# Kernel tuning notes

Hardware: AMD Instinct MI355X
Metric: run time of the kernel (lower is better)

Reference implementation:

```python
import jax, jax.numpy as jnp
import numpy as np

B, T, D, U, C = 256, 512, 128, 128, 64


def setup_inputs() -> dict:
    key = jax.random.key(0)
    ks = jax.random.split(key, 4)
    s_in = 1.0 / np.sqrt(D)
    s_u = 1.0 / np.sqrt(U)
    return {
        "inputs": jax.random.normal(ks[0], (B, T, D), dtype=jnp.float32),
        "W1": jax.random.normal(ks[1], (D, U), dtype=jnp.float32) * s_in,
        "b1": jnp.zeros((U,), dtype=jnp.float32),
        "W2": jax.random.normal(ks[2], (U, U), dtype=jnp.float32) * s_u,
        "b2": jnp.zeros((U,), dtype=jnp.float32),
        "Wc": jax.random.normal(ks[3], (U, C), dtype=jnp.float32) * s_u,
        "bc": jnp.zeros((C,), dtype=jnp.float32),
    }


def reference(inputs, W1, b1, W2, b2, Wc, bc):
    # state_{t} = tanh(x_t @ W1 + b1) + tanh(state_{t-1} @ W2 + b2)
    # Input projection has no recurrent dependency -> precompute in one big GEMM.
    h = jnp.tanh(jnp.einsum("btd,du->btu", inputs, W1) + b1)  # (B, T, U)

    def step(state, h_t):
        y = h_t + jnp.tanh(state @ W2 + b2)  # (B, U)
        return y, y

    state0 = jnp.zeros((inputs.shape[0], W2.shape[0]), dtype=inputs.dtype)
    _, ys = jax.lax.scan(step, state0, jnp.swapaxes(h, 0, 1))  # ys: (T, B, U)
    features = jnp.swapaxes(ys, 0, 1)  # (B, T, U)
    # classifier: Dense head applied to stacked features
    return jnp.einsum("btu,uc->btc", features, Wc) + bc
```

## Files before the change

kernel.cpp:

```cpp
#include <hip/hip_runtime.h>

#define NB 256
#define NT 512
#define ND 128
#define NU 128
#define NC 64
#define NM (NB * NT)
#define YP 136

typedef _Float16 half2v __attribute__((ext_vector_type(2)));
typedef _Float16 half4v __attribute__((ext_vector_type(4)));
typedef _Float16 half8v __attribute__((ext_vector_type(8)));
typedef float f32x4 __attribute__((ext_vector_type(4)));
typedef float v2f __attribute__((ext_vector_type(2)));

#define MFMA(a, b, c) __builtin_amdgcn_mfma_f32_16x16x32_f16((a), (b), (c), 0, 0, 0)

__device__ __forceinline__ half2v pk2(float a, float b) {
  return __builtin_bit_cast(half2v, __builtin_amdgcn_cvt_pkrtz(a, b));
}

__device__ __forceinline__ float tanh_s(float s) {
  float e = __expf(s);
  return fmaf(-2.0f, __builtin_amdgcn_rcpf(e + 1.0f), 1.0f);
}

__device__ __forceinline__ void wg_barrier() {
  asm volatile("s_waitcnt lgkmcnt(0)\n\ts_barrier" ::: "memory");
}

__global__ __launch_bounds__(256, 1) void k1_inproj(
    const float* __restrict__ x, const float* __restrict__ W1,
    const float* __restrict__ b1v, _Float16* __restrict__ TH)
{
  __shared__ _Float16 W1T[ND * YP];
  const int tid = (int)threadIdx.x;
  for (int i = tid; i < ND * NU; i += 256) {
    int k = i >> 7, n = i & 127;
    W1T[n * YP + k] = (_Float16)(2.0f * W1[i]);
  }
  __syncthreads();

  const int L = tid & 63, wv = tid >> 6;
  const int v = L & 15, q = L >> 4;
  const int m0 = (int)blockIdx.x * 64 + wv * 16;

  const float* xr = x + (size_t)(m0 + v) * ND + 8 * q;
  half8v xf[4];
#pragma unroll
  for (int kk = 0; kk < 4; ++kk) {
    float4 a = *(const float4*)(xr + 32 * kk);
    float4 b = *(const float4*)(xr + 32 * kk + 4);
    half2v p0 = pk2(a.x, a.y), p1 = pk2(a.z, a.w);
    half2v p2 = pk2(b.x, b.y), p3 = pk2(b.z, b.w);
    xf[kk] = (half8v){p0[0], p0[1], p1[0], p1[1], p2[0], p2[1], p3[0], p3[1]};
  }

#pragma unroll
  for (int ht = 0; ht < 8; ++ht) {
    f32x4 acc;
    {
      float4 bb = *(const float4*)&b1v[16 * ht + 4 * q];
      acc = (f32x4){2.f * bb.x, 2.f * bb.y, 2.f * bb.z, 2.f * bb.w};
    }
#pragma unroll
    for (int kk = 0; kk < 4; ++kk) {
      half8v wa = *(const half8v*)&W1T[(16 * ht + v) * YP + 32 * kk + 8 * q];
      acc = MFMA(wa, xf[kk], acc);
    }
    half2v zlo = pk2(tanh_s(acc[0]), tanh_s(acc[1]));
    half2v zhi = pk2(tanh_s(acc[2]), tanh_s(acc[3]));
    half4v z = {zlo[0], zlo[1], zhi[0], zhi[1]};
    *(half4v*)&TH[(size_t)(m0 + v) * NU + 16 * ht + 4 * q] = z;
  }
}

__global__ __launch_bounds__(512, 1) void k2_recur(
    const _Float16* __restrict__ TH, const float* __restrict__ W2,
    const float* __restrict__ b2v, _Float16* __restrict__ Yws)
{
  __shared__ _Float16 Ybuf[2][16 * YP];

  const int tid = (int)threadIdx.x;
  const int w = tid >> 6;
  const int L = tid & 63;
  const int v = L & 15, q = L >> 4;
  const int b0 = (int)blockIdx.x * 16;

  half8v w2f[4];
#pragma unroll
  for (int kk = 0; kk < 4; ++kk) {
    half8v h;
#pragma unroll
    for (int j = 0; j < 8; ++j)
      h[j] = (_Float16)(2.0f * W2[(size_t)(32 * kk + 8 * q + j) * NU + 16 * w + v]);
    w2f[kk] = h;
  }
  f32x4 b2f;
  {
    float4 bb = *(const float4*)&b2v[16 * w + 4 * q];
    b2f = (f32x4){2.f * bb.x, 2.f * bb.y, 2.f * bb.z, 2.f * bb.w};
  }

  const _Float16* thp = TH + (size_t)(b0 + v) * NT * NU + 16 * w + 4 * q;
  _Float16* yp = Yws + (size_t)(b0 + v) * NT * NU + 16 * w + 4 * q;

  half4v thr0 = *(const half4v*)(thp + 0 * NU);
  half4v thr1 = *(const half4v*)(thp + 1 * NU);
  half4v thr2 = *(const half4v*)(thp + 2 * NU);
  half4v thr3 = *(const half4v*)(thp + 3 * NU);

  f32x4 racc = b2f;
  _Float16* wr = &Ybuf[0][0] + v * YP + 16 * w + 4 * q;
  const _Float16* rd = &Ybuf[0][0] + v * YP + 8 * q;

#define K2STEP(T_, THR_, BUF_)                                                \
  {                                                                           \
    const int t_ = (T_);                                                      \
    half2v zlo = pk2(tanh_s(racc[0]), tanh_s(racc[1]));                       \
    half2v zhi = pk2(tanh_s(racc[2]), tanh_s(racc[3]));                       \
    half2v tlo = __builtin_shufflevector(THR_, THR_, 0, 1);                   \
    half2v thi = __builtin_shufflevector(THR_, THR_, 2, 3);                   \
    half2v ylo = zlo + tlo;                                                   \
    half2v yhi = zhi + thi;                                                   \
    half4v y4 = {ylo[0], ylo[1], yhi[0], yhi[1]};                             \
    *(half4v*)(wr + (BUF_) * (16 * YP)) = y4;                                 \
    *(half4v*)(yp + (size_t)t_ * NU) = y4;         \
    {                                                                         \
      int tn = t_ + 4; tn = tn < NT ? tn : NT - 1;                            \
      THR_ = *(const half4v*)(thp + (size_t)tn * NU);                         \
    }                                                                         \
    wg_barrier();                                                             \
    half8v yf0 = *(const half8v*)(rd + (BUF_) * (16 * YP) + 0);               \
    half8v yf1 = *(const half8v*)(rd + (BUF_) * (16 * YP) + 32);              \
    half8v yf2 = *(const half8v*)(rd + (BUF_) * (16 * YP) + 64);              \
    half8v yf3 = *(const half8v*)(rd + (BUF_) * (16 * YP) + 96);              \
    racc = b2f;                                                               \
    racc = MFMA(w2f[0], yf0, racc);                                           \
    racc = MFMA(w2f[1], yf1, racc);                                           \
    racc = MFMA(w2f[2], yf2, racc);                                           \
    racc = MFMA(w2f[3], yf3, racc);                                           \
  }

#pragma unroll 1
  for (int t = 0; t < NT; t += 4) {
    K2STEP(t + 0, thr0, 0)
    K2STEP(t + 1, thr1, 1)
    K2STEP(t + 2, thr2, 0)
    K2STEP(t + 3, thr3, 1)
  }
}

__global__ __launch_bounds__(256, 1) void k3_head(
    const _Float16* __restrict__ Y, const float* __restrict__ Wc,
    const float* __restrict__ bcv, float* __restrict__ out)
{
  __shared__ _Float16 WcT[NC * YP];
  const int tid = (int)threadIdx.x;
  for (int i = tid; i < NU * NC; i += 256) {
    int k = i >> 6, c = i & 63;
    WcT[c * YP + k] = (_Float16)Wc[i];
  }
  __syncthreads();

  const int L = tid & 63, wv = tid >> 6;
  const int v = L & 15, q = L >> 4;
  const int m0 = (int)blockIdx.x * 64 + wv * 16;

  const _Float16* yr = Y + (size_t)(m0 + v) * NU + 8 * q;
  half8v yf[4];
#pragma unroll
  for (int kk = 0; kk < 4; ++kk) yf[kk] = *(const half8v*)(yr + 32 * kk);

  float* op = out + (size_t)(m0 + v) * NC + 4 * q;
#pragma unroll
  for (int ct = 0; ct < 4; ++ct) {
    f32x4 acc;
    {
      float4 bb = *(const float4*)&bcv[16 * ct + 4 * q];
      acc = (f32x4){bb.x, bb.y, bb.z, bb.w};
    }
#pragma unroll
    for (int kk = 0; kk < 4; ++kk) {
      half8v wa = *(const half8v*)&WcT[(16 * ct + v) * YP + 32 * kk + 8 * q];
      acc = MFMA(wa, yf[kk], acc);
    }
    *(float4*)(op + 16 * ct) = (float4){acc[0], acc[1], acc[2], acc[3]};
  }
}

__device__ __forceinline__ float fast_tanh(float x) {
  float e = __expf(2.0f * x);
  return 1.0f - 2.0f / (e + 1.0f);
}
__device__ __forceinline__ float bcast(float val, int i) {
  return __builtin_bit_cast(float, __builtin_amdgcn_readlane(__builtin_bit_cast(int, val), i));
}

__global__ __launch_bounds__(256, 1) void rnn_fallback(
    const float* __restrict__ x, const float* __restrict__ W1,
    const float* __restrict__ b1v, const float* __restrict__ W2,
    const float* __restrict__ b2v, const float* __restrict__ Wc,
    const float* __restrict__ bcv, float* __restrict__ out)
{
  __shared__ float xring[16][ND];
  __shared__ float pH[2][4][NU];
  __shared__ float pR[2][4][NU];
  __shared__ float pC[2][4][NC];

  const int tid  = (int)threadIdx.x;
  const int lane = tid & 63;
  const int kg   = tid >> 6;
  const int b    = (int)blockIdx.x;
  const float4* xr4 = (const float4*)(x + (size_t)b * NT * ND);

  v2f w1f[32], w2f[32];
  float wcf[32];
#pragma unroll
  for (int i = 0; i < 32; ++i) {
    int k = kg * 32 + i;
    w1f[i] = (v2f){W1[k * NU + lane], W1[k * NU + lane + 64]};
    w2f[i] = (v2f){W2[k * NU + lane], W2[k * NU + lane + 64]};
    wcf[i] = Wc[k * NC + lane];
  }
  const float biasc = bcv[lane];
  float bias1 = 0.f, bias2 = 0.f;
  if (lane < 32) { bias1 = b1v[kg * 32 + lane]; bias2 = b2v[kg * 32 + lane]; }

  float4 stg = make_float4(0.f, 0.f, 0.f, 0.f);
  if (lane < 32) {
    float4 a0 = xr4[(kg + 0) * 32 + lane];
    float4 a1 = xr4[(kg + 4) * 32 + lane];
    ((float4*)xring[kg + 0])[lane] = a0;
    ((float4*)xring[kg + 4])[lane] = a1;
    stg = xr4[(kg + 8) * 32 + lane];
  }
  float yseg = 0.f;
  wg_barrier();

  for (int t = 0; t < NT; ++t) {
    const int pb = t & 1;
    v2f accH0 = {0.f, 0.f}, accH1 = {0.f, 0.f};
    const float4* xb = (const float4*)&xring[t & 15][kg * 32];
#pragma unroll
    for (int i = 0; i < 4; ++i) {
      float4 xa = xb[2 * i];
      float4 xc = xb[2 * i + 1];
      accH0 = w1f[8*i+0] * (v2f){xa.x, xa.x} + accH0;
      accH1 = w1f[8*i+1] * (v2f){xa.y, xa.y} + accH1;
      accH0 = w1f[8*i+2] * (v2f){xa.z, xa.z} + accH0;
      accH1 = w1f[8*i+3] * (v2f){xa.w, xa.w} + accH1;
      accH0 = w1f[8*i+4] * (v2f){xc.x, xc.x} + accH0;
      accH1 = w1f[8*i+5] * (v2f){xc.y, xc.y} + accH1;
      accH0 = w1f[8*i+6] * (v2f){xc.z, xc.z} + accH0;
      accH1 = w1f[8*i+7] * (v2f){xc.w, xc.w} + accH1;
    }
    v2f accH = accH0 + accH1;
    v2f accR0 = {0.f, 0.f}, accR1 = {0.f, 0.f};
    float accC0 = 0.f, accC1 = 0.f;
#pragma unroll
    for (int i = 0; i < 16; ++i) {
      float s0 = bcast(yseg, 2 * i);
      float s1 = bcast(yseg, 2 * i + 1);
      accR0 = w2f[2*i+0] * (v2f){s0, s0} + accR0;
      accR1 = w2f[2*i+1] * (v2f){s1, s1} + accR1;
      accC0 = fmaf(s0, wcf[2*i+0], accC0);
      accC1 = fmaf(s1, wcf[2*i+1], accC1);
    }
    v2f accR = accR0 + accR1;
    float accC = accC0 + accC1;

    pH[pb][kg][lane]      = accH.x;
    pH[pb][kg][lane + 64] = accH.y;
    pR[pb][kg][lane]      = accR.x;
    pR[pb][kg][lane + 64] = accR.y;
    pC[pb][kg][lane]      = accC;

    if (kg == (t & 3)) {
      if (lane < 32) {
        ((float4*)xring[(t + 8) & 15])[lane] = stg;
        int r = t + 12; r = (r < NT) ? r : (NT - 1);
        stg = xr4[r * 32 + lane];
      }
    }
    wg_barrier();
    if (lane < 32) {
      const int j = kg * 32 + lane;
      float hs = bias1, rs = bias2;
#pragma unroll
      for (int g = 0; g < 4; ++g) { hs += pH[pb][g][j]; rs += pR[pb][g][j]; }
      yseg = fast_tanh(hs) + fast_tanh(rs);
    }
    if (kg == ((t + 2) & 3) && t >= 1) {
      float cs = biasc;
#pragma unroll
      for (int g = 0; g < 4; ++g) cs += pC[pb][g][lane];
      out[((size_t)b * NT + (t - 1)) * NC + lane] = cs;
    }
  }
  float accC0 = 0.f, accC1 = 0.f;
#pragma unroll
  for (int i = 0; i < 16; ++i) {
    float s0 = bcast(yseg, 2 * i);
    float s1 = bcast(yseg, 2 * i + 1);
    accC0 = fmaf(s0, wcf[2*i+0], accC0);
    accC1 = fmaf(s1, wcf[2*i+1], accC1);
  }
  pC[0][kg][lane] = accC0 + accC1;
  wg_barrier();
  if (kg == 0) {
    float cs = biasc;
#pragma unroll
    for (int g = 0; g < 4; ++g) cs += pC[0][g][lane];
    out[((size_t)b * NT + (NT - 1)) * NC + lane] = cs;
  }
}

extern "C" void kernel_launch(void* const* d_in, const int* in_sizes, int n_in,
                              void* d_out, int out_size, void* d_ws, size_t ws_size,
                              hipStream_t stream) {
  (void)in_sizes; (void)n_in; (void)out_size;
  const float* x   = (const float*)d_in[0];
  const float* W1  = (const float*)d_in[1];
  const float* b1v = (const float*)d_in[2];
  const float* W2  = (const float*)d_in[3];
  const float* b2v = (const float*)d_in[4];
  const float* Wc  = (const float*)d_in[5];
  const float* bcv = (const float*)d_in[6];
  float* out = (float*)d_out;

  const size_t need = (size_t)NM * NU * 2 * 2;
  if (ws_size >= need) {
    _Float16* TH = (_Float16*)d_ws;
    _Float16* Yw = TH + (size_t)NM * NU;
    hipLaunchKernelGGL(k1_inproj, dim3(NM / 64), dim3(256), 0, stream, x, W1, b1v, TH);
    hipLaunchKernelGGL(k2_recur, dim3(NB / 16), dim3(512), 0, stream, TH, W2, b2v, Yw);
    hipLaunchKernelGGL(k3_head, dim3(NM / 64), dim3(256), 0, stream, Yw, Wc, bcv, out);
  } else {
    hipLaunchKernelGGL(rnn_fallback, dim3(NB), dim3(256), 0, stream,
                       x, W1, b1v, W2, b2v, Wc, bcv, out);
  }
}
```

Baseline: 311.0 us.

## Fuse classifier head into recurrence kernel and use exp2-scaled tanh

The classifier head GEMM moves into the recurrent kernel: four of the eight waves multiply each step's Y tile by Wc held in registers and write fp32 outputs directly. This removes the fp16 Y workspace round-trip and the third kernel launch. Weights are prescaled by 2/ln2 so tanh uses exp2 directly, and the h_t addition is folded into the final FMA in fp32. The recurrent MFMA chain is split into two accumulators to shorten dependency latency, and the TH prefetch distance is deepened. In exchange the serial recurrent loop does extra head MFMAs and global stores on half the waves each step.

```diff
diff --git a/kernel.cpp b/kernel.cpp
--- a/kernel.cpp
+++ b/kernel.cpp
@@ -7,6 +7,7 @@
 #define NC 64
 #define NM (NB * NT)
 #define YP 136
+#define SCL 2.8853900817779268f
 
 typedef _Float16 half2v __attribute__((ext_vector_type(2)));
 typedef _Float16 half4v __attribute__((ext_vector_type(4)));
@@ -21,8 +22,12 @@
 }
 
 __device__ __forceinline__ float tanh_s(float s) {
-  float e = __expf(s);
+  float e = __builtin_amdgcn_exp2f(s);
   return fmaf(-2.0f, __builtin_amdgcn_rcpf(e + 1.0f), 1.0f);
+}
+__device__ __forceinline__ float ytanh(float s, float u) {
+  float e = __builtin_amdgcn_exp2f(s);
+  return fmaf(-2.0f, __builtin_amdgcn_rcpf(e + 1.0f), u);
 }
 
 __device__ __forceinline__ void wg_barrier() {
@@ -35,9 +40,11 @@
 {
   __shared__ _Float16 W1T[ND * YP];
   const int tid = (int)threadIdx.x;
-  for (int i = tid; i < ND * NU; i += 256) {
-    int k = i >> 7, n = i & 127;
-    W1T[n * YP + k] = (_Float16)(2.0f * W1[i]);
+  for (int i = tid; i < ND * NU / 2; i += 256) {
+    int n = i & 127, kh = i >> 7;
+    half2v p = {(_Float16)(SCL * W1[(size_t)(2 * kh) * NU + n]),
+                (_Float16)(SCL * W1[(size_t)(2 * kh + 1) * NU + n])};
+    *(half2v*)&W1T[n * YP + 2 * kh] = p;
   }
   __syncthreads();
 
@@ -61,7 +68,7 @@
     f32x4 acc;
     {
       float4 bb = *(const float4*)&b1v[16 * ht + 4 * q];
-      acc = (f32x4){2.f * bb.x, 2.f * bb.y, 2.f * bb.z, 2.f * bb.w};
+      acc = (f32x4){SCL * bb.x, SCL * bb.y, SCL * bb.z, SCL * bb.w};
     }
 #pragma unroll
     for (int kk = 0; kk < 4; ++kk) {
@@ -77,7 +84,8 @@
 
 __global__ __launch_bounds__(512, 1) void k2_recur(
     const _Float16* __restrict__ TH, const float* __restrict__ W2,
-    const float* __restrict__ b2v, _Float16* __restrict__ Yws)
+    const float* __restrict__ b2v, const float* __restrict__ Wc,
+    const float* __restrict__ bcv, float* __restrict__ out)
 {
   __shared__ _Float16 Ybuf[2][16 * YP];
 
@@ -93,100 +101,99 @@
     half8v h;
 #pragma unroll
     for (int j = 0; j < 8; ++j)
-      h[j] = (_Float16)(2.0f * W2[(size_t)(32 * kk + 8 * q + j) * NU + 16 * w + v]);
+      h[j] = (_Float16)(SCL * W2[(size_t)(32 * kk + 8 * q + j) * NU + 16 * w + v]);
     w2f[kk] = h;
   }
   f32x4 b2f;
   {
     float4 bb = *(const float4*)&b2v[16 * w + 4 * q];
-    b2f = (f32x4){2.f * bb.x, 2.f * bb.y, 2.f * bb.z, 2.f * bb.w};
+    b2f = (f32x4){SCL * bb.x, SCL * bb.y, SCL * bb.z, SCL * bb.w};
+  }
+
+  const bool whead = (w < 4);
+  half8v wcf[4];
+  f32x4 bcf = (f32x4){0.f, 0.f, 0.f, 0.f};
+  float* op = out;
+  if (whead) {
+#pragma unroll
+    for (int kk = 0; kk < 4; ++kk) {
+      half8v h;
+#pragma unroll
+      for (int j = 0; j < 8; ++j)
+        h[j] = (_Float16)Wc[(size_t)(32 * kk + 8 * q + j) * NC + 16 * w + v];
+      wcf[kk] = h;
+    }
+    float4 bb = *(const float4*)&bcv[16 * w + 4 * q];
+    bcf = (f32x4){bb.x, bb.y, bb.z, bb.w};
+    op = out + (size_t)(b0 + v) * NT * NC + 16 * w + 4 * q;
   }
 
   const _Float16* thp = TH + (size_t)(b0 + v) * NT * NU + 16 * w + 4 * q;
-  _Float16* yp = Yws + (size_t)(b0 + v) * NT * NU + 16 * w + 4 * q;
-
-  half4v thr0 = *(const half4v*)(thp + 0 * NU);
-  half4v thr1 = *(const half4v*)(thp + 1 * NU);
-  half4v thr2 = *(const half4v*)(thp + 2 * NU);
-  half4v thr3 = *(const half4v*)(thp + 3 * NU);
+
+#define CVTU(A)                                                               \
+  (f32x4){1.f + (float)(A)[0], 1.f + (float)(A)[1],                           \
+          1.f + (float)(A)[2], 1.f + (float)(A)[3]}
+
+  f32x4 uf0, uf1, uf2, uf3;
+  {
+    half4v a0 = *(const half4v*)(thp + 0 * NU);
+    half4v a1 = *(const half4v*)(thp + 1 * NU);
+    half4v a2 = *(const half4v*)(thp + 2 * NU);
+    half4v a3 = *(const half4v*)(thp + 3 * NU);
+    uf0 = CVTU(a0); uf1 = CVTU(a1); uf2 = CVTU(a2); uf3 = CVTU(a3);
+  }
+  half4v thr0 = *(const half4v*)(thp + 4 * NU);
+  half4v thr1 = *(const half4v*)(thp + 5 * NU);
+  half4v thr2 = *(const half4v*)(thp + 6 * NU);
+  half4v thr3 = *(const half4v*)(thp + 7 * NU);
 
   f32x4 racc = b2f;
   _Float16* wr = &Ybuf[0][0] + v * YP + 16 * w + 4 * q;
   const _Float16* rd = &Ybuf[0][0] + v * YP + 8 * q;
-
-#define K2STEP(T_, THR_, BUF_)                                                \
+  const f32x4 zero4 = (f32x4){0.f, 0.f, 0.f, 0.f};
+
+#define K2STEP(T_, UF_, THR_, BUF_)                                           \
   {                                                                           \
     const int t_ = (T_);                                                      \
-    half2v zlo = pk2(tanh_s(racc[0]), tanh_s(racc[1]));                       \
-    half2v zhi = pk2(tanh_s(racc[2]), tanh_s(racc[3]));                       \
-    half2v tlo = __builtin_shufflevector(THR_, THR_, 0, 1);                   \
-    half2v thi = __builtin_shufflevector(THR_, THR_, 2, 3);                   \
-    half2v ylo = zlo + tlo;                                                   \
-    half2v yhi = zhi + thi;                                                   \
+    half2v ylo = pk2(ytanh(racc[0], UF_[0]), ytanh(racc[1], UF_[1]));         \
+    half2v yhi = pk2(ytanh(racc[2], UF_[2]), ytanh(racc[3], UF_[3]));         \
     half4v y4 = {ylo[0], ylo[1], yhi[0], yhi[1]};                             \
     *(half4v*)(wr + (BUF_) * (16 * YP)) = y4;                                 \
-    *(half4v*)(yp + (size_t)t_ * NU) = y4;         \
-    {                                                                         \
-      int tn = t_ + 4; tn = tn < NT ? tn : NT - 1;                            \
-      THR_ = *(const half4v*)(thp + (size_t)tn * NU);                         \
-    }                                                                         \
     wg_barrier();                                                             \
     half8v yf0 = *(const half8v*)(rd + (BUF_) * (16 * YP) + 0);               \
     half8v yf1 = *(const half8v*)(rd + (BUF_) * (16 * YP) + 32);              \
     half8v yf2 = *(const half8v*)(rd + (BUF_) * (16 * YP) + 64);              \
     half8v yf3 = *(const half8v*)(rd + (BUF_) * (16 * YP) + 96);              \
-    racc = b2f;                                                               \
-    racc = MFMA(w2f[0], yf0, racc);                                           \
-    racc = MFMA(w2f[1], yf1, racc);                                           \
-    racc = MFMA(w2f[2], yf2, racc);                                           \
-    racc = MFMA(w2f[3], yf3, racc);                                           \
+    f32x4 ra = MFMA(w2f[0], yf0, b2f);          \
+    f32x4 rb = MFMA(w2f[1], yf1, zero4);                                      \
+    ra = MFMA(w2f[2], yf2, ra);                                               \
+    rb = MFMA(w2f[3], yf3, rb);                                               \
+    if (whead) {                                                              \
+      f32x4 oacc = bcf;                                                       \
+      oacc = MFMA(wcf[0], yf0, oacc);                                         \
+      oacc = MFMA(wcf[1], yf1, oacc);                                         \
+      oacc = MFMA(wcf[2], yf2, oacc);                                         \
+      oacc = MFMA(wcf[3], yf3, oacc);                                         \
+      *(float4*)(op + (size_t)t_ * NC) =                                      \
+          (float4){oacc[0], oacc[1], oacc[2], oacc[3]};                       \
+    }                                                                         \
+    {                                                                         \
+      UF_ = CVTU(THR_);      \
+      int tn = t_ + 8; tn = tn < NT ? tn : NT - 1;                            \
+      THR_ = *(const half4v*)(thp + (size_t)tn * NU);                         \
+    }                                                                         \
+    racc = ra + rb;                                                           \
   }
 
 #pragma unroll 1
   for (int t = 0; t < NT; t += 4) {
-    K2STEP(t + 0, thr0, 0)
-    K2STEP(t + 1, thr1, 1)
-    K2STEP(t + 2, thr2, 0)
-    K2STEP(t + 3, thr3, 1)
-  }
-}
-
-__global__ __launch_bounds__(256, 1) void k3_head(
-    const _Float16* __restrict__ Y, const float* __restrict__ Wc,
-    const float* __restrict__ bcv, float* __restrict__ out)
-{
-  __shared__ _Float16 WcT[NC * YP];
-  const int tid = (int)threadIdx.x;
-  for (int i = tid; i < NU * NC; i += 256) {
-    int k = i >> 6, c = i & 63;
-    WcT[c * YP + k] = (_Float16)Wc[i];
-  }
-  __syncthreads();
-
-  const int L = tid & 63, wv = tid >> 6;
-  const int v = L & 15, q = L >> 4;
-  const int m0 = (int)blockIdx.x * 64 + wv * 16;
-
-  const _Float16* yr = Y + (size_t)(m0 + v) * NU + 8 * q;
-  half8v yf[4];
-#pragma unroll
-  for (int kk = 0; kk < 4; ++kk) yf[kk] = *(const half8v*)(yr + 32 * kk);
-
-  float* op = out + (size_t)(m0 + v) * NC + 4 * q;
-#pragma unroll
-  for (int ct = 0; ct < 4; ++ct) {
-    f32x4 acc;
-    {
-      float4 bb = *(const float4*)&bcv[16 * ct + 4 * q];
-      acc = (f32x4){bb.x, bb.y, bb.z, bb.w};
-    }
-#pragma unroll
-    for (int kk = 0; kk < 4; ++kk) {
-      half8v wa = *(const half8v*)&WcT[(16 * ct + v) * YP + 32 * kk + 8 * q];
-      acc = MFMA(wa, yf[kk], acc);
-    }
-    *(float4*)(op + 16 * ct) = (float4){acc[0], acc[1], acc[2], acc[3]};
-  }
+    K2STEP(t + 0, uf0, thr0, 0)
+    K2STEP(t + 1, uf1, thr1, 1)
+    K2STEP(t + 2, uf2, thr2, 0)
+    K2STEP(t + 3, uf3, thr3, 1)
+  }
+#undef K2STEP
+#undef CVTU
 }
 
 __device__ __forceinline__ float fast_tanh(float x) {
@@ -329,13 +336,12 @@
   const float* bcv = (const float*)d_in[6];
   float* out = (float*)d_out;
 
-  const size_t need = (size_t)NM * NU * 2 * 2;
+  const size_t need = (size_t)NM * NU * 2;
   if (ws_size >= need) {
     _Float16* TH = (_Float16*)d_ws;
-    _Float16* Yw = TH + (size_t)NM * NU;
     hipLaunchKernelGGL(k1_inproj, dim3(NM / 64), dim3(256), 0, stream, x, W1, b1v, TH);
-    hipLaunchKernelGGL(k2_recur, dim3(NB / 16), dim3(512), 0, stream, TH, W2, b2v, Yw);
-    hipLaunchKernelGGL(k3_head, dim3(NM / 64), dim3(256), 0, stream, Yw, Wc, bcv, out);
+    hipLaunchKernelGGL(k2_recur, dim3(NB / 16), dim3(512), 0, stream,
+                       TH, W2, b2v, Wc, bcv, out);
   } else {
     hipLaunchKernelGGL(rnn_fallback, dim3(NB), dim3(256), 0, stream,
                        x, W1, b1v, W2, b2v, Wc, bcv, out);
```

Result: slower. 318.5 us (+2.4%).
